# Kernel optimization log

Hardware: AMD Instinct MI355X
Metric: run time of the kernel (lower is better)

The kernel has to match this reference:

```python
import jax, jax.numpy as jnp
import numpy as np

INPUT_DIM = 1024
EMBED_DIMS = 128


def setup_inputs() -> dict:
    key = jax.random.key(0)
    ks = jax.random.split(key, 7)
    s_in = 1.0 / np.sqrt(INPUT_DIM)
    x = jax.random.normal(ks[0], (4, 4096, INPUT_DIM), dtype=jnp.float32)
    Wq = jax.random.uniform(ks[1], (INPUT_DIM, EMBED_DIMS), jnp.float32, -s_in, s_in)
    bq = jax.random.uniform(ks[2], (EMBED_DIMS,), jnp.float32, -s_in, s_in)
    Wk = jax.random.uniform(ks[3], (INPUT_DIM, EMBED_DIMS), jnp.float32, -s_in, s_in)
    bk = jax.random.uniform(ks[4], (EMBED_DIMS,), jnp.float32, -s_in, s_in)
    Wv = jax.random.uniform(ks[5], (INPUT_DIM, EMBED_DIMS), jnp.float32, -s_in, s_in)
    bv = jax.random.uniform(ks[6], (EMBED_DIMS,), jnp.float32, -s_in, s_in)
    return {"x": x, "Wq": Wq, "bq": bq, "Wk": Wk, "bk": bk, "Wv": Wv, "bv": bv}


def reference(x, Wq, bq, Wk, bk, Wv, bv):
    # x: [B, L, C]
    Q = jnp.einsum('blc,cd->bld', x, Wq) + bq  # [B, L, D]
    K = jnp.einsum('blc,cd->bld', x, Wk) + bk
    V = jnp.einsum('blc,cd->bld', x, Wv) + bv
    d_k = Q.shape[-1]
    scores = jnp.einsum('bld,bmd->blm', Q, K) / jnp.sqrt(jnp.float32(d_k))  # [B, L, L]
    attn = jax.nn.softmax(scores, axis=-1)
    return jnp.einsum('blm,bmd->bld', attn, V)  # [B, L, D]
```

## Files before the change

kernel.cpp:

```cpp
#include <hip/hip_runtime.h>
#include <stdint.h>

typedef __bf16 bf16;
typedef __bf16 bf16x8 __attribute__((ext_vector_type(8)));
typedef __bf16 bf16x4 __attribute__((ext_vector_type(4)));
typedef _Float16 f16;
typedef f16 f16x8 __attribute__((ext_vector_type(8)));
typedef f16 f16x4 __attribute__((ext_vector_type(4)));
typedef float f32x16 __attribute__((ext_vector_type(16)));
typedef uint32_t u32x4 __attribute__((ext_vector_type(4)));

#define LQ    16384
#define CDIM  1024
#define DDIM  128
#define NSPLIT 4
#define QS 0.12751741f

static __device__ __forceinline__ uint32_t pkrtz(float a, float b) {
  return __builtin_bit_cast(uint32_t, __builtin_amdgcn_cvt_pkrtz(a, b));
}

static __device__ __forceinline__ void lds_barrier() {
  asm volatile("s_waitcnt lgkmcnt(0)" ::: "memory");
  __builtin_amdgcn_s_barrier();
}

static __device__ __forceinline__ void gload_lds16(const void* g, void* l) {
  __builtin_amdgcn_global_load_lds(
      (__attribute__((address_space(1))) void*)g,
      (__attribute__((address_space(3))) void*)l, 16, 0, 0);
}

__global__ void prep_kernel(const float* __restrict__ Wq, const float* __restrict__ Wk,
                            const float* __restrict__ Wv, const float* __restrict__ bq,
                            const float* __restrict__ bk, const float* __restrict__ bv,
                            bf16* __restrict__ Wt, float* __restrict__ bias_all) {
  int idx = blockIdx.x * 256 + threadIdx.x;
  int p = idx >> 17;
  int rem = idx & 131071;
  int k = rem >> 7, n = rem & 127;
  const float* W = (p == 0) ? Wq : (p == 1) ? Wk : Wv;
  float s = (p == 0) ? QS : 1.0f;
  Wt[(size_t)(p * 128 + n) * CDIM + k] = (bf16)(W[rem] * s);
  if (idx < 384) {
    int pp = idx >> 7, nn = idx & 127;
    const float* b = (pp == 0) ? bq : (pp == 1) ? bk : bv;
    bias_all[idx] = b[nn] * ((pp == 0) ? QS : 1.0f);
  }
}

__global__ __launch_bounds__(512, 1) void qkv_gemm(
    const float* __restrict__ x, const bf16* __restrict__ Wt,
    const float* __restrict__ bias_all,
    bf16* __restrict__ Qw, bf16* __restrict__ Kw, f16* __restrict__ Vtw) {
  __shared__ bf16 As[2][64 * 64];
  __shared__ bf16 Bs[2][384 * 64];
  const int t = threadIdx.x;
  const int w = t >> 6;
  const int lane = t & 63;
  const int l31 = lane & 31;
  const int hi = lane >> 5;
  const int m0 = blockIdx.x * 64;
  const int m_off = (w & 1) * 32;
  const int n_off = ((w >> 1) & 3) * 32;

  const f32x16 z16 = {0.f,0.f,0.f,0.f,0.f,0.f,0.f,0.f,0.f,0.f,0.f,0.f,0.f,0.f,0.f,0.f};
  f32x16 acc[3];
  acc[0] = z16; acc[1] = z16; acc[2] = z16;

  const int srow = t >> 3;
  const int g = t & 7;
  const int sgoff = (g ^ (srow & 7)) * 8;
  const int scol = g * 8;

  const int lrow = lane >> 3;
  const int lgr = (lane & 7) ^ lrow;
  const bf16* bsrc = Wt + (size_t)(w * 48 + lrow) * CDIM + lgr * 8;

  float4 xa[2];
  {
    const float* p = &x[(size_t)(m0 + srow) * CDIM + scol];
    xa[0] = *(const float4*)p;
    xa[1] = *(const float4*)(p + 4);
  }
#pragma unroll
  for (int c = 0; c < 6; c++)
    gload_lds16(bsrc + (size_t)c * 8 * CDIM, &Bs[0][(w * 48 + c * 8) * 64]);
  {
    bf16x8 v;
    v[0] = (bf16)xa[0].x; v[1] = (bf16)xa[0].y;
    v[2] = (bf16)xa[0].z; v[3] = (bf16)xa[0].w;
    v[4] = (bf16)xa[1].x; v[5] = (bf16)xa[1].y;
    v[6] = (bf16)xa[1].z; v[7] = (bf16)xa[1].w;
    *(bf16x8*)&As[0][srow * 64 + sgoff] = v;
  }
  lds_barrier();

  for (int kc = 0; kc < 16; kc++) {
    bf16* Ab = As[kc & 1];
    bf16* Bb = Bs[kc & 1];

    if (kc < 15) {
      const bf16* s = bsrc + (kc + 1) * 64;
      bf16* Bn = Bs[(kc + 1) & 1];
#pragma unroll
      for (int c = 0; c < 6; c++)
        gload_lds16(s + (size_t)c * 8 * CDIM, &Bn[(w * 48 + c * 8) * 64]);
      const float* p = &x[(size_t)(m0 + srow) * CDIM + (kc + 1) * 64 + scol];
      xa[0] = *(const float4*)p;
      xa[1] = *(const float4*)(p + 4);
    }

#pragma unroll
    for (int ks = 0; ks < 4; ks++) {
      const int rg = ((ks * 2 + hi) ^ (l31 & 7)) * 8;
      bf16x8 af = *(const bf16x8*)&Ab[(m_off + l31) * 64 + rg];
#pragma unroll
      for (int p = 0; p < 3; p++) {
        bf16x8 bfr = *(const bf16x8*)&Bb[(p * 128 + n_off + l31) * 64 + rg];
        acc[p] = __builtin_amdgcn_mfma_f32_32x32x16_bf16(af, bfr, acc[p], 0, 0, 0);
      }
    }

    if (kc < 15) {
      bf16* An = As[(kc + 1) & 1];
      bf16x8 v;
      v[0] = (bf16)xa[0].x; v[1] = (bf16)xa[0].y;
      v[2] = (bf16)xa[0].z; v[3] = (bf16)xa[0].w;
      v[4] = (bf16)xa[1].x; v[5] = (bf16)xa[1].y;
      v[6] = (bf16)xa[1].z; v[7] = (bf16)xa[1].w;
      *(bf16x8*)&An[srow * 64 + sgoff] = v;
      lds_barrier();
    }
  }

  const int n = n_off + l31;
#pragma unroll
  for (int p = 0; p < 3; p++) {
    const float bias = bias_all[p * 128 + n];
    if (p < 2) {
      bf16* outp = (p == 0) ? Qw : Kw;
#pragma unroll
      for (int r = 0; r < 16; r++) {
        int m = m0 + m_off + (r & 3) + 8 * (r >> 2) + 4 * hi;
        outp[(size_t)m * DDIM + n] = (bf16)(acc[p][r] + bias);
      }
    } else {
#pragma unroll
      for (int gq = 0; gq < 4; gq++) {
        int mbase = m0 + m_off + 8 * gq + 4 * hi;
        f16x4 pv;
#pragma unroll
        for (int r = 0; r < 4; r++) pv[r] = (f16)(acc[p][gq * 4 + r] + bias);
        *(f16x4*)&Vtw[(size_t)n * LQ + mbase] = pv;
      }
    }
  }
}

__global__ __launch_bounds__(256, 2) void flash_kernel(
    const bf16* __restrict__ Qw, const bf16* __restrict__ Kw, const f16* __restrict__ Vtw,
    bf16* __restrict__ Opb, float* __restrict__ lp) {
  __shared__ bf16 Kl[2][64 * 136];
  __shared__ f16  Vl[2][128 * 72];

  const int t = threadIdx.x;
  const int w = t >> 6;
  const int lane = t & 63;
  const int l31 = lane & 31;
  const int hi = lane >> 5;
  const int lin = blockIdx.y * 128 + blockIdx.x;
  const int logical = ((lin & 7) << 6) + (lin >> 3);
  const int qb = logical & 127;
  const int sp = logical >> 7;
  const int batch = qb >> 5;
  const int q0w = qb * 128 + w * 32;
  const int kv_base = batch * 4096 + sp * 1024;

  bf16x8 qf[8];
#pragma unroll
  for (int ks = 0; ks < 8; ks++)
    qf[ks] = *(const bf16x8*)&Qw[(size_t)(q0w + l31) * DDIM + ks * 16 + hi * 8];

  const f32x16 z16 = {0.f,0.f,0.f,0.f,0.f,0.f,0.f,0.f,0.f,0.f,0.f,0.f,0.f,0.f,0.f,0.f};
  f32x16 o[4];
  o[0] = z16; o[1] = z16; o[2] = z16; o[3] = z16;
  f32x16 liacc = z16;

  f16x8 ones;
#pragma unroll
  for (int i = 0; i < 8; i++) ones[i] = (f16)1.f;

  const int kr = t >> 4;
  const int kcol = (t & 15) << 3;
  const int vr = t >> 3;
  const int vcol = (t & 7) << 3;

  bf16x8 ka[4];
  f16x8 va[4];
  f16x8 pa[4];

#pragma unroll
  for (int c = 0; c < 4; c++)
    ka[c] = *(const bf16x8*)&Kw[(size_t)(kv_base + c * 16 + kr) * DDIM + kcol];
#pragma unroll
  for (int c = 0; c < 4; c++)
    va[c] = *(const f16x8*)&Vtw[(size_t)(c * 32 + vr) * LQ + kv_base + vcol];

#pragma unroll
  for (int c = 0; c < 4; c++)
    *(bf16x8*)&Kl[0][(c * 16 + kr) * 136 + kcol] = ka[c];
#pragma unroll
  for (int c = 0; c < 4; c++)
    *(f16x8*)&Vl[0][(c * 32 + vr) * 72 + vcol] = va[c];

#pragma unroll
  for (int c = 0; c < 4; c++)
    ka[c] = *(const bf16x8*)&Kw[(size_t)(kv_base + 64 + c * 16 + kr) * DDIM + kcol];
#pragma unroll
  for (int c = 0; c < 4; c++)
    va[c] = *(const f16x8*)&Vtw[(size_t)(c * 32 + vr) * LQ + kv_base + 64 + vcol];

  lds_barrier();

  f32x16 sv0 = z16, sv1 = z16;
  __builtin_amdgcn_s_setprio(1);
#pragma unroll
  for (int ks = 0; ks < 8; ks++) {
    bf16x8 kf0 = *(const bf16x8*)&Kl[0][l31 * 136 + ks * 16 + hi * 8];
    bf16x8 kf1 = *(const bf16x8*)&Kl[0][(32 + l31) * 136 + ks * 16 + hi * 8];
    sv0 = __builtin_amdgcn_mfma_f32_32x32x16_bf16(kf0, qf[ks], sv0, 0, 0, 0);
    sv1 = __builtin_amdgcn_mfma_f32_32x32x16_bf16(kf1, qf[ks], sv1, 0, 0, 0);
  }
  __builtin_amdgcn_s_setprio(0);
#pragma unroll
  for (int r = 0; r < 16; r++) {
    sv0[r] = __builtin_amdgcn_exp2f(sv0[r]);
    sv1[r] = __builtin_amdgcn_exp2f(sv1[r]);
  }
#pragma unroll
  for (int sl = 0; sl < 4; sl++) {
    const int b = (sl & 1) * 8;
    float s0 = (sl >> 1) ? sv1[b + 0] : sv0[b + 0];
    float s1 = (sl >> 1) ? sv1[b + 1] : sv0[b + 1];
    float s2 = (sl >> 1) ? sv1[b + 2] : sv0[b + 2];
    float s3 = (sl >> 1) ? sv1[b + 3] : sv0[b + 3];
    float s4 = (sl >> 1) ? sv1[b + 4] : sv0[b + 4];
    float s5 = (sl >> 1) ? sv1[b + 5] : sv0[b + 5];
    float s6 = (sl >> 1) ? sv1[b + 6] : sv0[b + 6];
    float s7 = (sl >> 1) ? sv1[b + 7] : sv0[b + 7];
    uint32_t a0 = pkrtz(s0, s1);
    uint32_t a1 = pkrtz(s2, s3);
    uint32_t a2 = pkrtz(s4, s5);
    uint32_t a3 = pkrtz(s6, s7);
    asm("v_permlane32_swap_b32 %0, %1" : "+v"(a0), "+v"(a2));
    asm("v_permlane32_swap_b32 %0, %1" : "+v"(a1), "+v"(a3));
    u32x4 aw; aw.x = a0; aw.y = a1; aw.z = a2; aw.w = a3;
    pa[sl] = __builtin_bit_cast(f16x8, aw);
  }

  for (int tile = 0; tile < 15; tile++) {
    bf16* Kb = Kl[(tile + 1) & 1];
    f16*  Vb = Vl[(tile + 1) & 1];
    f16*  Vp = Vl[tile & 1];
#pragma unroll
    for (int c = 0; c < 4; c++)
      *(bf16x8*)&Kb[(c * 16 + kr) * 136 + kcol] = ka[c];
#pragma unroll
    for (int c = 0; c < 4; c++)
      *(f16x8*)&Vb[(c * 32 + vr) * 72 + vcol] = va[c];

    const int kvn = kv_base + (tile < 14 ? tile + 2 : 15) * 64;
#pragma unroll
    for (int c = 0; c < 4; c++)
      ka[c] = *(const bf16x8*)&Kw[(size_t)(kvn + c * 16 + kr) * DDIM + kcol];
#pragma unroll
    for (int c = 0; c < 4; c++)
      va[c] = *(const f16x8*)&Vtw[(size_t)(c * 32 + vr) * LQ + kvn + vcol];

    lds_barrier();

    sv0 = z16; sv1 = z16;
    __builtin_amdgcn_s_setprio(1);
#pragma unroll
    for (int i = 0; i < 4; i++) {
      bf16x8 kf0a = *(const bf16x8*)&Kb[l31 * 136 + (2 * i) * 16 + hi * 8];
      bf16x8 kf1a = *(const bf16x8*)&Kb[(32 + l31) * 136 + (2 * i) * 16 + hi * 8];
      bf16x8 kf0b = *(const bf16x8*)&Kb[l31 * 136 + (2 * i + 1) * 16 + hi * 8];
      bf16x8 kf1b = *(const bf16x8*)&Kb[(32 + l31) * 136 + (2 * i + 1) * 16 + hi * 8];
      sv0 = __builtin_amdgcn_mfma_f32_32x32x16_bf16(kf0a, qf[2 * i], sv0, 0, 0, 0);
      sv1 = __builtin_amdgcn_mfma_f32_32x32x16_bf16(kf1a, qf[2 * i], sv1, 0, 0, 0);
      const int koff = (i >> 1) * 32 + (i & 1) * 16 + hi * 8;
#pragma unroll
      for (int dt = 0; dt < 4; dt++) {
        f16x8 vf = *(const f16x8*)&Vp[(dt * 32 + l31) * 72 + koff];
        o[dt] = __builtin_amdgcn_mfma_f32_32x32x16_f16(pa[i], vf, o[dt], 0, 0, 0);
      }
      liacc = __builtin_amdgcn_mfma_f32_32x32x16_f16(pa[i], ones, liacc, 0, 0, 0);
      sv0 = __builtin_amdgcn_mfma_f32_32x32x16_bf16(kf0b, qf[2 * i + 1], sv0, 0, 0, 0);
      sv1 = __builtin_amdgcn_mfma_f32_32x32x16_bf16(kf1b, qf[2 * i + 1], sv1, 0, 0, 0);
    }
    __builtin_amdgcn_s_setprio(0);

#pragma unroll
    for (int r = 0; r < 16; r++) {
      sv0[r] = __builtin_amdgcn_exp2f(sv0[r]);
      sv1[r] = __builtin_amdgcn_exp2f(sv1[r]);
    }
#pragma unroll
    for (int sl = 0; sl < 4; sl++) {
      const int b = (sl & 1) * 8;
      float s0 = (sl >> 1) ? sv1[b + 0] : sv0[b + 0];
      float s1 = (sl >> 1) ? sv1[b + 1] : sv0[b + 1];
      float s2 = (sl >> 1) ? sv1[b + 2] : sv0[b + 2];
      float s3 = (sl >> 1) ? sv1[b + 3] : sv0[b + 3];
      float s4 = (sl >> 1) ? sv1[b + 4] : sv0[b + 4];
      float s5 = (sl >> 1) ? sv1[b + 5] : sv0[b + 5];
      float s6 = (sl >> 1) ? sv1[b + 6] : sv0[b + 6];
      float s7 = (sl >> 1) ? sv1[b + 7] : sv0[b + 7];
      uint32_t a0 = pkrtz(s0, s1);
      uint32_t a1 = pkrtz(s2, s3);
      uint32_t a2 = pkrtz(s4, s5);
      uint32_t a3 = pkrtz(s6, s7);
      asm("v_permlane32_swap_b32 %0, %1" : "+v"(a0), "+v"(a2));
      asm("v_permlane32_swap_b32 %0, %1" : "+v"(a1), "+v"(a3));
      u32x4 aw; aw.x = a0; aw.y = a1; aw.z = a2; aw.w = a3;
      pa[sl] = __builtin_bit_cast(f16x8, aw);
    }

    __builtin_amdgcn_s_barrier();
  }

  {
    f16* Vp = Vl[15 & 1];
    __builtin_amdgcn_s_setprio(1);
#pragma unroll
    for (int i = 0; i < 4; i++) {
      const int koff = (i >> 1) * 32 + (i & 1) * 16 + hi * 8;
#pragma unroll
      for (int dt = 0; dt < 4; dt++) {
        f16x8 vf = *(const f16x8*)&Vp[(dt * 32 + l31) * 72 + koff];
        o[dt] = __builtin_amdgcn_mfma_f32_32x32x16_f16(pa[i], vf, o[dt], 0, 0, 0);
      }
      liacc = __builtin_amdgcn_mfma_f32_32x32x16_f16(pa[i], ones, liacc, 0, 0, 0);
    }
    __builtin_amdgcn_s_setprio(0);
  }

  const size_t po = (size_t)sp * LQ * DDIM;
#pragma unroll
  for (int dt = 0; dt < 4; dt++)
#pragma unroll
    for (int r = 0; r < 16; r++) {
      int q = q0w + (r & 3) + 8 * (r >> 2) + 4 * hi;
      Opb[po + (size_t)q * DDIM + dt * 32 + l31] = (bf16)o[dt][r];
    }
  if (l31 == 0) {
#pragma unroll
    for (int r = 0; r < 16; r++)
      lp[(size_t)sp * LQ + q0w + (r & 3) + 8 * (r >> 2) + 4 * hi] = liacc[r];
  }
}

__global__ void combine_kernel(const bf16* __restrict__ Opb, const float* __restrict__ lp,
                               float* __restrict__ out) {
  int idx = blockIdx.x * 256 + threadIdx.x;
  int q = idx >> 5;
  int d = (idx & 31) * 4;
  float lsum = 0.f;
  float acc[4] = {0.f, 0.f, 0.f, 0.f};
#pragma unroll
  for (int sp = 0; sp < NSPLIT; sp++) {
    lsum += lp[(size_t)sp * LQ + q];
    bf16x4 ov = *(const bf16x4*)&Opb[(size_t)sp * LQ * DDIM + (size_t)q * DDIM + d];
#pragma unroll
    for (int j = 0; j < 4; j++) acc[j] += (float)ov[j];
  }
  float inv = 1.0f / lsum;
  float4 r;
  r.x = acc[0] * inv; r.y = acc[1] * inv; r.z = acc[2] * inv; r.w = acc[3] * inv;
  *(float4*)&out[(size_t)q * DDIM + d] = r;
}

extern "C" void kernel_launch(void* const* d_in, const int* in_sizes, int n_in,
                              void* d_out, int out_size, void* d_ws, size_t ws_size,
                              hipStream_t stream) {
  const float* x  = (const float*)d_in[0];
  const float* Wq = (const float*)d_in[1];
  const float* bq = (const float*)d_in[2];
  const float* Wk = (const float*)d_in[3];
  const float* bk = (const float*)d_in[4];
  const float* Wv = (const float*)d_in[5];
  const float* bv = (const float*)d_in[6];
  char* ws = (char*)d_ws;
  bf16* Qw   = (bf16*)(ws);
  bf16* Kw   = (bf16*)(ws + ((size_t)4 << 20));
  f16*  Vtw  = (f16*)(ws + ((size_t)8 << 20));
  bf16* Wt   = (bf16*)(ws + ((size_t)12 << 20));
  float* bias_all = (float*)(ws + ((size_t)12 << 20) + 786432);
  bf16* Opb  = (bf16*)(ws + ((size_t)13 << 20));
  float* lpp = (float*)(ws + ((size_t)29 << 20));
  float* out = (float*)d_out;

  prep_kernel<<<1536, 256, 0, stream>>>(Wq, Wk, Wv, bq, bk, bv, Wt, bias_all);
  qkv_gemm<<<256, 512, 0, stream>>>(x, Wt, bias_all, Qw, Kw, Vtw);
  flash_kernel<<<dim3(128, NSPLIT), 256, 0, stream>>>(Qw, Kw, Vtw, Opb, lpp);
  combine_kernel<<<2048, 256, 0, stream>>>(Opb, lpp, out);
}
```

Baseline: 170.9 us.

## Prefetch x two chunks ahead in projection; compute softmax row sums with VALU

```diff
diff --git a/kernel.cpp b/kernel.cpp
--- a/kernel.cpp
+++ b/kernel.cpp
@@ -77,22 +77,24 @@
   const int lgr = (lane & 7) ^ lrow;
   const bf16* bsrc = Wt + (size_t)(w * 48 + lrow) * CDIM + lgr * 8;
 
-  float4 xa[2];
-  {
-    const float* p = &x[(size_t)(m0 + srow) * CDIM + scol];
-    xa[0] = *(const float4*)p;
-    xa[1] = *(const float4*)(p + 4);
-  }
+  float4 xc0, xc1, xn0, xn1;
+
 #pragma unroll
   for (int c = 0; c < 6; c++)
     gload_lds16(bsrc + (size_t)c * 8 * CDIM, &Bs[0][(w * 48 + c * 8) * 64]);
   {
+    const float* p = &x[(size_t)(m0 + srow) * CDIM + scol];
+    float4 a0 = *(const float4*)p;
+    float4 a1 = *(const float4*)(p + 4);
     bf16x8 v;
-    v[0] = (bf16)xa[0].x; v[1] = (bf16)xa[0].y;
-    v[2] = (bf16)xa[0].z; v[3] = (bf16)xa[0].w;
-    v[4] = (bf16)xa[1].x; v[5] = (bf16)xa[1].y;
-    v[6] = (bf16)xa[1].z; v[7] = (bf16)xa[1].w;
+    v[0] = (bf16)a0.x; v[1] = (bf16)a0.y; v[2] = (bf16)a0.z; v[3] = (bf16)a0.w;
+    v[4] = (bf16)a1.x; v[5] = (bf16)a1.y; v[6] = (bf16)a1.z; v[7] = (bf16)a1.w;
     *(bf16x8*)&As[0][srow * 64 + sgoff] = v;
+  }
+  {
+    const float* p = &x[(size_t)(m0 + srow) * CDIM + 64 + scol];
+    xc0 = *(const float4*)p;
+    xc1 = *(const float4*)(p + 4);
   }
   lds_barrier();
 
@@ -106,9 +108,12 @@
 #pragma unroll
       for (int c = 0; c < 6; c++)
         gload_lds16(s + (size_t)c * 8 * CDIM, &Bn[(w * 48 + c * 8) * 64]);
-      const float* p = &x[(size_t)(m0 + srow) * CDIM + (kc + 1) * 64 + scol];
-      xa[0] = *(const float4*)p;
-      xa[1] = *(const float4*)(p + 4);
+      __builtin_amdgcn_sched_barrier(0);
+      if (kc < 14) {
+        const float* p = &x[(size_t)(m0 + srow) * CDIM + (kc + 2) * 64 + scol];
+        xn0 = *(const float4*)p;
+        xn1 = *(const float4*)(p + 4);
+      }
     }
 
 #pragma unroll
@@ -125,12 +130,16 @@
     if (kc < 15) {
       bf16* An = As[(kc + 1) & 1];
       bf16x8 v;
-      v[0] = (bf16)xa[0].x; v[1] = (bf16)xa[0].y;
-      v[2] = (bf16)xa[0].z; v[3] = (bf16)xa[0].w;
-      v[4] = (bf16)xa[1].x; v[5] = (bf16)xa[1].y;
-      v[6] = (bf16)xa[1].z; v[7] = (bf16)xa[1].w;
+      v[0] = (bf16)xc0.x; v[1] = (bf16)xc0.y; v[2] = (bf16)xc0.z; v[3] = (bf16)xc0.w;
+      v[4] = (bf16)xc1.x; v[5] = (bf16)xc1.y; v[6] = (bf16)xc1.z; v[7] = (bf16)xc1.w;
       *(bf16x8*)&An[srow * 64 + sgoff] = v;
+      __builtin_amdgcn_sched_barrier(0);
+      if (kc < 14)
+        asm volatile("s_waitcnt vmcnt(2)" ::: "memory");
+      else
+        asm volatile("s_waitcnt vmcnt(0)" ::: "memory");
       lds_barrier();
+      xc0 = xn0; xc1 = xn1;
     }
   }
 
@@ -185,11 +194,7 @@
   const f32x16 z16 = {0.f,0.f,0.f,0.f,0.f,0.f,0.f,0.f,0.f,0.f,0.f,0.f,0.f,0.f,0.f,0.f};
   f32x16 o[4];
   o[0] = z16; o[1] = z16; o[2] = z16; o[3] = z16;
-  f32x16 liacc = z16;
-
-  f16x8 ones;
-#pragma unroll
-  for (int i = 0; i < 8; i++) ones[i] = (f16)1.f;
+  float lsum = 0.f;
 
   const int kr = t >> 4;
   const int kcol = (t & 15) << 3;
@@ -237,6 +242,14 @@
   for (int r = 0; r < 16; r++) {
     sv0[r] = __builtin_amdgcn_exp2f(sv0[r]);
     sv1[r] = __builtin_amdgcn_exp2f(sv1[r]);
+  }
+  {
+    float ts = 0.f;
+#pragma unroll
+    for (int r = 0; r < 16; r++) ts += sv0[r] + sv1[r];
+    float xsw = ts, ysw = ts;
+    asm("v_permlane32_swap_b32 %0, %1" : "+v"(xsw), "+v"(ysw));
+    lsum += xsw + ysw;
   }
 #pragma unroll
   for (int sl = 0; sl < 4; sl++) {
@@ -296,7 +309,6 @@
         f16x8 vf = *(const f16x8*)&Vp[(dt * 32 + l31) * 72 + koff];
         o[dt] = __builtin_amdgcn_mfma_f32_32x32x16_f16(pa[i], vf, o[dt], 0, 0, 0);
       }
-      liacc = __builtin_amdgcn_mfma_f32_32x32x16_f16(pa[i], ones, liacc, 0, 0, 0);
       sv0 = __builtin_amdgcn_mfma_f32_32x32x16_bf16(kf0b, qf[2 * i + 1], sv0, 0, 0, 0);
       sv1 = __builtin_amdgcn_mfma_f32_32x32x16_bf16(kf1b, qf[2 * i + 1], sv1, 0, 0, 0);
     }
@@ -306,6 +318,14 @@
     for (int r = 0; r < 16; r++) {
       sv0[r] = __builtin_amdgcn_exp2f(sv0[r]);
       sv1[r] = __builtin_amdgcn_exp2f(sv1[r]);
+    }
+    {
+      float ts = 0.f;
+#pragma unroll
+      for (int r = 0; r < 16; r++) ts += sv0[r] + sv1[r];
+      float xsw = ts, ysw = ts;
+      asm("v_permlane32_swap_b32 %0, %1" : "+v"(xsw), "+v"(ysw));
+      lsum += xsw + ysw;
     }
 #pragma unroll
     for (int sl = 0; sl < 4; sl++) {
@@ -342,7 +362,6 @@
         f16x8 vf = *(const f16x8*)&Vp[(dt * 32 + l31) * 72 + koff];
         o[dt] = __builtin_amdgcn_mfma_f32_32x32x16_f16(pa[i], vf, o[dt], 0, 0, 0);
       }
-      liacc = __builtin_amdgcn_mfma_f32_32x32x16_f16(pa[i], ones, liacc, 0, 0, 0);
     }
     __builtin_amdgcn_s_setprio(0);
   }
@@ -355,11 +374,8 @@
       int q = q0w + (r & 3) + 8 * (r >> 2) + 4 * hi;
       Opb[po + (size_t)q * DDIM + dt * 32 + l31] = (bf16)o[dt][r];
     }
-  if (l31 == 0) {
-#pragma unroll
-    for (int r = 0; r < 16; r++)
-      lp[(size_t)sp * LQ + q0w + (r & 3) + 8 * (r >> 2) + 4 * hi] = liacc[r];
-  }
+  if (hi == 0)
+    lp[(size_t)sp * LQ + q0w + l31] = lsum;
 }
 
 __global__ void combine_kernel(const bf16* __restrict__ Opb, const float* __restrict__ lp,
```

Measured after the change: 168.7 us. Within noise of the previous version (-1.3%).
